# Kernel tuning notes

Hardware: AMD Instinct MI355X
Metric: run time of the kernel (lower is better)

The kernel has to match this reference:

```python
import jax, jax.numpy as jnp
import numpy as np

B = 8          # batch
S = 256        # nx+1 = ny+1 grid resolution
N = S * S      # number of DoFs per component
DIM = 2        # output vector dimension (= d_out)
W = 32         # FNO channel width
M1 = 12        # Fourier modes dim 1
M2 = 12        # Fourier modes dim 2
WF = 128       # final MLP hidden width
NL = 4         # number of Fourier layers
PADF = 8       # padding fraction denominator


def setup_inputs() -> dict:
    key = jax.random.key(0)
    ks = jax.random.split(key, 16)
    sc = 1.0 / (W * W)  # torch FNO spectral weight init scale
    return {
        "x": jax.random.normal(ks[0], (B, N), jnp.float32),
        "d2v_in": jax.random.permutation(ks[1], jnp.arange(N)),
        "v2d_out": jax.random.permutation(ks[2], jnp.arange(N)),
        "fc0_w": jax.random.normal(ks[3], (W, 3), jnp.float32) * 0.1,
        "fc0_b": jnp.zeros((W,), jnp.float32),
        "spec_w1r": jax.random.uniform(ks[4], (NL, W, W, M1, M2), jnp.float32) * sc,
        "spec_w1i": jax.random.uniform(ks[5], (NL, W, W, M1, M2), jnp.float32) * sc,
        "spec_w2r": jax.random.uniform(ks[6], (NL, W, W, M1, M2), jnp.float32) * sc,
        "spec_w2i": jax.random.uniform(ks[7], (NL, W, W, M1, M2), jnp.float32) * sc,
        "conv_w": jax.random.normal(ks[8], (NL, W, W), jnp.float32) * 0.05,
        "conv_b": jnp.zeros((NL, W), jnp.float32),
        "mlp_w1": jax.random.normal(ks[9], (WF, W), jnp.float32) * 0.05,
        "mlp_b1": jnp.zeros((WF,), jnp.float32),
        "mlp_w2": jax.random.normal(ks[10], (DIM, WF), jnp.float32) * 0.05,
        "mlp_b2": jnp.zeros((DIM,), jnp.float32),
    }


def _speconv(x, w1, w2):
    # x: (B, C, H, Wd) real; w1/w2: (C_in, C_out, M1, M2) complex64
    Bh, C, H, Wd = x.shape
    xft = jnp.fft.rfft2(x)  # (B, C, H, Wd//2+1)
    o1 = jnp.einsum('bixy,ioxy->boxy', xft[:, :, :M1, :M2], w1)
    o2 = jnp.einsum('bixy,ioxy->boxy', xft[:, :, -M1:, :M2], w2)
    out_ft = jnp.zeros((Bh, C, H, Wd // 2 + 1), jnp.complex64)
    out_ft = out_ft.at[:, :, :M1, :M2].set(o1).at[:, :, -M1:, :M2].set(o2)
    return jnp.fft.irfft2(out_ft, s=(H, Wd))


def reference(x, d2v_in, v2d_out, fc0_w, fc0_b,
              spec_w1r, spec_w1i, spec_w2r, spec_w2i,
              conv_w, conv_b, mlp_w1, mlp_b1, mlp_w2, mlp_b2):
    # DoF -> vertex gather and lift to image
    xg = x[:, d2v_in].reshape(B, 1, S, S)
    h = jnp.transpose(xg, (0, 2, 3, 1))  # (B, S, S, 1)
    # append normalized grid coordinates (get_grid2d)
    g = jnp.linspace(0.0, 1.0, S, dtype=jnp.float32)
    grid = jnp.stack(jnp.meshgrid(g, g, indexing='ij'), axis=-1)  # (S, S, 2)
    grid = jnp.broadcast_to(grid[None], (B, S, S, 2))
    h = jnp.concatenate([h, grid], axis=-1)
    # fc0 lifting
    h = h @ fc0_w.T + fc0_b              # (B, S, S, W)
    h = jnp.transpose(h, (0, 3, 1, 2))   # (B, W, S, S)
    # zero pad (non-periodic domain)
    p = S // PADF
    h = jnp.pad(h, ((0, 0), (0, 0), (0, p), (0, p)))  # (B, W, S+p, S+p)
    w1 = (spec_w1r + 1j * spec_w1i).astype(jnp.complex64)
    w2 = (spec_w2r + 1j * spec_w2i).astype(jnp.complex64)
    for l in range(NL):
        sp = _speconv(h, w1[l], w2[l])
        cv = jnp.einsum('bchw,oc->bohw', h, conv_w[l]) + conv_b[l][None, :, None, None]
        h = cv + sp
        if l != NL - 1:
            h = jax.nn.gelu(h, approximate=False)  # torch GELU default = exact erf
    # crop padding (s_outputspace=None path)
    h = h[..., :S, :S]
    # final two-layer MLP projection
    h = jnp.transpose(h, (0, 2, 3, 1))  # (B, S, S, W)
    h = jax.nn.gelu(h @ mlp_w1.T + mlp_b1, approximate=False) @ mlp_w2.T + mlp_b2
    h = jnp.transpose(h, (0, 3, 1, 2)).reshape(B, DIM, -1)  # (B, DIM, N)
    # vertex -> DoF scatter/gather and interleave components
    out = h[:, :, v2d_out]              # (B, DIM, N)
    out = jnp.transpose(out, (0, 2, 1)).reshape(B, -1)  # (B, N*DIM)
    return out
```

## Files before the change

kernel.cpp:

```cpp
#include <hip/hip_runtime.h>
#include <math.h>

#define S    256
#define Hp   288
#define C    32
#define KY   12
#define NK   24
#define Bn   8
#define PI_D 3.14159265358979323846264338327950288

#define SZ_TW  (NK*Hp*2)
#define OFF_TW 0
#define OFF_TWT (OFF_TW + SZ_TW)
#define SZ_TWT (Hp*KY*2)
#define OFF_H  (OFF_TWT + SZ_TWT)
#define SZ_H   (Bn*C*Hp*Hp)
#define OFF_Y  (OFF_H + SZ_H)
#define SZ_Y   (Bn*C*Hp*KY*2)
#define OFF_X  (OFF_Y + SZ_Y)
#define SZ_X   (Bn*C*NK*KY*2)
#define OFF_O  (OFF_X + 2*SZ_X)
#define SZ_O   SZ_X
#define OFF_Z  (OFF_O + SZ_O)
#define SZ_Z   (Bn*Hp*C*KY*2)
#define OFF_T  (OFF_Z + SZ_Z)
#define SZ_T   (Bn*S*S*2)

#define GELU(v) (0.5f*(v)*(1.0f+erff((v)*0.70710678118654752f)))
#define SCHED_FENCE() __builtin_amdgcn_sched_barrier(0)

__global__ void k_tw(float* __restrict__ tw, float* __restrict__ twT) {
    int i = blockIdx.x * 256 + threadIdx.x;
    if (i >= NK * Hp) return;
    int k = i / Hp, xx = i % Hp;
    int f = (k < KY) ? k : (k + 264);
    int m = (f * xx) % Hp;
    double th = (2.0 * PI_D * (double)m) / (double)Hp;
    float c = (float)cos(th), s = (float)sin(th);
    tw[2 * i] = c; tw[2 * i + 1] = s;
    if (k < KY) { twT[xx * 24 + 2 * k] = c; twT[xx * 24 + 2 * k + 1] = s; }
}

template<int Q>
__device__ __forceinline__ void embed_body(
        const float* __restrict__ xs, const float* __restrict__ twq,
        float* __restrict__ h, size_t rowbase, int o, int g,
        float w0, float w1, float w2, float bb, float gx,
        float* pr, float* pi) {
    #pragma unroll 1
    for (int c3 = 0; c3 < 3; ++c3) {
        int ybase = g * 36 + c3 * 12;
        int rowq  = (g & 1) * 36 + c3 * 12;
        float acc[12];
        #pragma unroll
        for (int j = 0; j < 12; ++j) {
            int y = ybase + j;
            acc[j] = (y < S) ? (w0 * xs[y < S ? y : 0] + w1 * gx + w2 * (y * (1.0f / 255.0f)) + bb) : 0.f;
        }
        float* hw = h + rowbase + (size_t)o * 82944 + ybase;
        #pragma unroll
        for (int q = 0; q < 3; ++q)
            *(float4*)&hw[4 * q] = make_float4(acc[4*q], acc[4*q+1], acc[4*q+2], acc[4*q+3]);
        SCHED_FENCE();
        #pragma unroll
        for (int jp = 0; jp < 6; ++jp) {
            #pragma unroll
            for (int u = 0; u < 2; ++u) {
                int j = jp * 2 + u;
                const float* tg = twq + (rowq + j) * 24;
                float tc[24];
                #pragma unroll
                for (int q = 0; q < 6; ++q) *(float4*)&tc[4 * q] = *(const float4*)&tg[4 * q];
                float v = acc[j];
                pr[0] += v;
                #pragma unroll
                for (int k = 1; k < 12; ++k) {
                    const int e = (k * Q) & 3;
                    float c = tc[2 * k], s = tc[2 * k + 1];
                    if      (e == 0) { pr[k] += v * c; pi[k] -= v * s; }
                    else if (e == 1) { pr[k] -= v * s; pi[k] -= v * c; }
                    else if (e == 2) { pr[k] -= v * c; pi[k] += v * s; }
                    else             { pr[k] += v * s; pi[k] += v * c; }
                }
            }
            SCHED_FENCE();
        }
    }
}

__global__ __launch_bounds__(256, 1) void k_embed(
        const float* __restrict__ xin, const int* __restrict__ d2v,
        const float* __restrict__ fw, const float* __restrict__ fb,
        const float* __restrict__ twT, float* __restrict__ h, float* __restrict__ Y) {
    __shared__ __align__(16) float xs[256];
    __shared__ __align__(16) float twq[1728];
    __shared__ __align__(16) float YP[3072];
    int x = blockIdx.x, b = blockIdx.y, tid = threadIdx.x;
    size_t rowbase = (size_t)b * 2654208 + (size_t)x * 288;
    if (x >= S) {
        for (int i = tid; i < 32 * 72; i += 256) {
            int c = i / 72, q = i % 72;
            *(float4*)&h[rowbase + (size_t)c * 82944 + q * 4] = make_float4(0, 0, 0, 0);
        }
        for (int i = tid; i < 768; i += 256)
            Y[((size_t)(b * 32 + i / 24) * 288 + x) * 24 + (i % 24)] = 0.f;
        return;
    }
    for (int i = tid; i < 432; i += 256)
        *(float4*)&twq[4 * i] = *(const float4*)&twT[4 * i];
    xs[tid] = xin[b * 65536 + d2v[x * 256 + tid]];
    int o = tid & 31, g = tid >> 5;
    float w0 = fw[o * 3], w1 = fw[o * 3 + 1], w2 = fw[o * 3 + 2], bb = fb[o];
    float gx = x * (1.0f / 255.0f);
    __syncthreads();
    float pr[12], pi[12];
    #pragma unroll
    for (int k = 0; k < 12; ++k) { pr[k] = 0.f; pi[k] = 0.f; }
    switch (tid >> 6) {
        case 0: embed_body<0>(xs, twq, h, rowbase, o, g, w0, w1, w2, bb, gx, pr, pi); break;
        case 1: embed_body<1>(xs, twq, h, rowbase, o, g, w0, w1, w2, bb, gx, pr, pi); break;
        case 2: embed_body<2>(xs, twq, h, rowbase, o, g, w0, w1, w2, bb, gx, pr, pi); break;
        default: embed_body<3>(xs, twq, h, rowbase, o, g, w0, w1, w2, bb, gx, pr, pi); break;
    }
    #pragma unroll
    for (int k = 0; k < 12; ++k) { pr[k] += __shfl_xor(pr[k], 32); pi[k] += __shfl_xor(pi[k], 32); }
    if ((tid & 32) == 0) {
        float* dst = YP + ((tid >> 6) * 32 + o) * 24;
        #pragma unroll
        for (int k = 0; k < 12; ++k) { dst[2 * k] = pr[k]; dst[2 * k + 1] = pi[k]; }
    }
    __syncthreads();
    for (int i = tid; i < 768; i += 256) {
        float s = YP[i] + YP[768 + i] + YP[1536 + i] + YP[2304 + i];
        Y[((size_t)(b * 32 + i / 24) * 288 + x) * 24 + (i % 24)] = s;
    }
}

__global__ __launch_bounds__(288) void k_dftx(const float* __restrict__ Y,
                                              const float* __restrict__ tw,
                                              float* __restrict__ X) {
    __shared__ __align__(16) float Ys[144 * 24];
    int c = blockIdx.x, b = blockIdx.y, half = blockIdx.z, tid = threadIdx.x;
    const float* Yb = Y + (size_t)(b * 32 + c) * 6912 + half * 3456;
    for (int i = tid; i < 864; i += 288)
        *(float4*)&Ys[4 * i] = *(const float4*)&Yb[4 * i];
    __syncthreads();
    int k = tid / 12, ky = tid % 12;
    const float* twk = tw + k * 576 + half * 288;
    float xr = 0.f, xi = 0.f;
    #pragma unroll 4
    for (int xx = 0; xx < 144; ++xx) {
        float yr = Ys[xx * 24 + 2 * ky], yi = Ys[xx * 24 + 2 * ky + 1];
        float cc = twk[2 * xx], ss = twk[2 * xx + 1];
        xr += yr * cc + yi * ss;
        xi += yi * cc - yr * ss;
    }
    size_t oo = (size_t)half * SZ_X + ((size_t)(b * 32 + c) * 288 + tid) * 2;
    X[oo] = xr; X[oo + 1] = xi;
}

__global__ void k_spec(const float* __restrict__ X,
                       const float* __restrict__ w1r, const float* __restrict__ w1i,
                       const float* __restrict__ w2r, const float* __restrict__ w2i,
                       float* __restrict__ O, int l) {
    int t = blockIdx.x * 256 + threadIdx.x;
    int ky = t % KY; int k = (t / KY) % NK; int o = (t / (NK * KY)) % C; int b = t / (C * NK * KY);
    int kk = (k < KY) ? k : (k - KY);
    const float* wr = (k < KY) ? w1r : w2r;
    const float* wi = (k < KY) ? w1i : w2i;
    size_t wbase = (size_t)l * C * C * 144 + (size_t)o * 144 + kk * 12 + ky;
    size_t xbase = (size_t)b * C * NK * KY * 2 + (k * KY + ky) * 2;
    float ar = 0.f, ai = 0.f;
    #pragma unroll 8
    for (int i = 0; i < C; ++i) {
        size_t xo = xbase + (size_t)i * NK * KY * 2;
        float xr = X[xo]     + X[SZ_X + xo];
        float xi = X[xo + 1] + X[SZ_X + xo + 1];
        float wrr = wr[wbase + (size_t)i * C * 144];
        float wii = wi[wbase + (size_t)i * C * 144];
        ar += xr * wrr - xi * wii;
        ai += xr * wii + xi * wrr;
    }
    size_t oo = (((size_t)b * C + o) * NK * KY + k * KY + ky) * 2;
    O[oo] = ar; O[oo + 1] = ai;
}

__global__ __launch_bounds__(384) void k_idftx(const float* __restrict__ O,
                                               const float* __restrict__ tw,
                                               float* __restrict__ Z) {
    int x0 = blockIdx.x * 32; int c = blockIdx.y, b = blockIdx.z;
    int row = threadIdx.x & 31, ky = threadIdx.x >> 5;
    int x = x0 + row;
    const float* Ob = O + ((size_t)(b * C + c)) * NK * KY * 2 + ky * 2;
    float zr = 0.f, zi = 0.f;
    #pragma unroll
    for (int k = 0; k < NK; ++k) {
        float orr = Ob[k * KY * 2], oii = Ob[k * KY * 2 + 1];
        float cc = tw[(k * Hp + x) * 2], ss = tw[(k * Hp + x) * 2 + 1];
        zr += orr * cc - oii * ss;
        zi += orr * ss + oii * cc;
    }
    size_t o = ((((size_t)b * Hp + x) * C + c) * KY + ky) * 2;
    Z[o] = zr; Z[o + 1] = zi;
}

__global__ __launch_bounds__(256, 1) void k_conv(
        float* __restrict__ h, const float* __restrict__ Z,
        const float* __restrict__ cw, const float* __restrict__ cb,
        const float* __restrict__ twT, float* __restrict__ Y,
        int l, int flags) {
    __shared__ __align__(16) float hs[32 * 292];
    __shared__ __align__(16) float twy[288 * 24];
    __shared__ __align__(16) float cws[32 * 33];
    __shared__ float cbs[32];
    int x = blockIdx.x, b = blockIdx.y, tid = threadIdx.x;
    size_t rowbase = (size_t)b * 2654208 + (size_t)x * 288;
    const float* hb = h + rowbase;
    for (int i = tid; i < 32 * 72; i += 256) {
        int c = i / 72, q = i % 72;
        *(float4*)&hs[c * 292 + q * 4] = *(const float4*)&hb[(size_t)c * 82944 + q * 4];
    }
    for (int i = tid; i < 1728; i += 256)
        *(float4*)&twy[4 * i] = *(const float4*)&twT[4 * i];
    for (int i = tid; i < 32 * 32; i += 256)
        cws[(i >> 5) * 33 + (i & 31)] = cw[l * 1024 + i];
    if (tid < 32) cbs[tid] = cb[l * 32 + tid];
    int o = tid & 31, g = tid >> 5;
    const float* Zr = Z + ((size_t)(b * 288 + x) * 32 + o) * 24;
    float zr[12], zi[12];
    #pragma unroll
    for (int q = 0; q < 6; ++q) {
        float4 zv = *(const float4*)&Zr[4 * q];
        zr[2*q] = zv.x; zi[2*q] = zv.y; zr[2*q+1] = zv.z; zi[2*q+1] = zv.w;
    }
    __syncthreads();
    float bias = cbs[o];
    float pr[12], pi[12];
    #pragma unroll
    for (int k = 0; k < 12; ++k) { pr[k] = 0.f; pi[k] = 0.f; }
    const int gelu_f = flags & 1, wy = flags & 2;
    #pragma unroll 1
    for (int c3 = 0; c3 < 3; ++c3) {
        int ybase = g * 36 + c3 * 12;
        float acc[12];
        #pragma unroll
        for (int j = 0; j < 12; ++j) acc[j] = bias;
        #pragma unroll 8
        for (int c = 0; c < 32; ++c) {
            float w = cws[o * 33 + c];
            const float* hr = &hs[c * 292 + ybase];
            float4 h0 = *(const float4*)&hr[0];
            float4 h1 = *(const float4*)&hr[4];
            float4 h2 = *(const float4*)&hr[8];
            acc[0] += h0.x * w; acc[1] += h0.y * w; acc[2]  += h0.z * w; acc[3]  += h0.w * w;
            acc[4] += h1.x * w; acc[5] += h1.y * w; acc[6]  += h1.z * w; acc[7]  += h1.w * w;
            acc[8] += h2.x * w; acc[9] += h2.y * w; acc[10] += h2.z * w; acc[11] += h2.w * w;
        }
        SCHED_FENCE();
        #pragma unroll
        for (int jp = 0; jp < 6; ++jp) {
            #pragma unroll
            for (int u = 0; u < 2; ++u) {
                int j = jp * 2 + u;
                int y = ybase + j;
                float tc[24];
                #pragma unroll
                for (int q = 0; q < 6; ++q) *(float4*)&tc[4 * q] = *(const float4*)&twy[y * 24 + 4 * q];
                float sp = zr[0] * tc[0] - zi[0] * tc[1];
                #pragma unroll
                for (int k = 1; k < 12; ++k) sp += 2.f * (zr[k] * tc[2*k] - zi[k] * tc[2*k+1]);
                float val = acc[j] + sp * (1.0f / 82944.0f);
                if (gelu_f) val = GELU(val);
                acc[j] = val;
                if (wy) {
                    #pragma unroll
                    for (int k = 0; k < 12; ++k) { pr[k] += val * tc[2*k]; pi[k] -= val * tc[2*k+1]; }
                }
            }
            SCHED_FENCE();
        }
        float* hw = h + rowbase + (size_t)o * 82944 + ybase;
        #pragma unroll
        for (int q = 0; q < 3; ++q)
            *(float4*)&hw[4 * q] = make_float4(acc[4*q], acc[4*q+1], acc[4*q+2], acc[4*q+3]);
        SCHED_FENCE();
    }
    if (wy) {
        #pragma unroll
        for (int k = 0; k < 12; ++k) { pr[k] += __shfl_xor(pr[k], 32); pi[k] += __shfl_xor(pi[k], 32); }
        __syncthreads();
        float* YP = twy;
        if ((tid & 32) == 0) {
            float* dst = YP + ((tid >> 6) * 32 + o) * 24;
            #pragma unroll
            for (int k = 0; k < 12; ++k) { dst[2 * k] = pr[k]; dst[2 * k + 1] = pi[k]; }
        }
        __syncthreads();
        for (int i = tid; i < 768; i += 256) {
            float s = YP[i] + YP[768 + i] + YP[1536 + i] + YP[2304 + i];
            Y[((size_t)(b * 32 + i / 24) * 288 + x) * 24 + (i % 24)] = s;
        }
    }
}

__global__ __launch_bounds__(256) void k_mlp(const float* __restrict__ h,
                                             const float* __restrict__ w1, const float* __restrict__ b1,
                                             const float* __restrict__ w2, const float* __restrict__ b2,
                                             float* __restrict__ tmp) {
    int bid = blockIdx.x;
    int b = bid >> 7;
    int x = ((bid & 127) << 1) + (threadIdx.x >> 7);
    int lane = threadIdx.x & 127;
    const float* hb = h + (size_t)b * 2654208 + (size_t)x * 288;
    float hc0[32], hc1[32];
    #pragma unroll
    for (int c = 0; c < 32; ++c) {
        hc0[c] = hb[(size_t)c * 82944 + lane];
        hc1[c] = hb[(size_t)c * 82944 + lane + 128];
    }
    float o00 = 0.f, o01 = 0.f, o10 = 0.f, o11 = 0.f;
    for (int f = 0; f < 128; ++f) {
        float a0 = b1[f], a1 = a0;
        #pragma unroll
        for (int c = 0; c < 32; ++c) {
            float w = w1[f * 32 + c];
            a0 += hc0[c] * w; a1 += hc1[c] * w;
        }
        float wa = w2[f], wb = w2[128 + f];
        float g0 = GELU(a0), g1 = GELU(a1);
        o00 += g0 * wa; o01 += g0 * wb;
        o10 += g1 * wa; o11 += g1 * wb;
    }
    float bb0 = b2[0], bb1 = b2[1];
    int p0 = x * 256 + lane;
    size_t base = (size_t)b * 65536;
    *(float2*)&tmp[(base + p0) * 2]       = make_float2(o00 + bb0, o01 + bb1);
    *(float2*)&tmp[(base + p0 + 128) * 2] = make_float2(o10 + bb0, o11 + bb1);
}

__global__ void k_scatter(const float* __restrict__ tmp, const int* __restrict__ v2d,
                          float* __restrict__ out) {
    int id = blockIdx.x * 256 + threadIdx.x;
    int b = id >> 16; int j = id & 65535;
    int p = v2d[j];
    const float2 v = *(const float2*)(tmp + ((size_t)(b << 16) + p) * 2);
    *(float2*)(out + (size_t)id * 2) = v;
}

extern "C" void kernel_launch(void* const* d_in, const int* in_sizes, int n_in,
                              void* d_out, int out_size, void* d_ws, size_t ws_size,
                              hipStream_t stream) {
    const float* xin   = (const float*)d_in[0];
    const int*   d2v   = (const int*)  d_in[1];
    const int*   v2d   = (const int*)  d_in[2];
    const float* fc0w  = (const float*)d_in[3];
    const float* fc0b  = (const float*)d_in[4];
    const float* w1r   = (const float*)d_in[5];
    const float* w1i   = (const float*)d_in[6];
    const float* w2r   = (const float*)d_in[7];
    const float* w2i   = (const float*)d_in[8];
    const float* cw    = (const float*)d_in[9];
    const float* cb    = (const float*)d_in[10];
    const float* mw1   = (const float*)d_in[11];
    const float* mb1   = (const float*)d_in[12];
    const float* mw2   = (const float*)d_in[13];
    const float* mb2   = (const float*)d_in[14];

    float* ws  = (float*)d_ws;
    float* TW  = ws + OFF_TW;
    float* TWT = ws + OFF_TWT;
    float* H   = ws + OFF_H;
    float* Y   = ws + OFF_Y;
    float* X   = ws + OFF_X;
    float* O   = ws + OFF_O;
    float* Z   = ws + OFF_Z;
    float* T   = ws + OFF_T;

    k_tw<<<(NK * Hp + 255) / 256, 256, 0, stream>>>(TW, TWT);
    k_embed<<<dim3(Hp, Bn), 256, 0, stream>>>(xin, d2v, fc0w, fc0b, TWT, H, Y);

    for (int l = 0; l < 4; ++l) {
        k_dftx<<<dim3(32, Bn, 2), 288, 0, stream>>>(Y, TW, X);
        k_spec<<<(Bn * C * NK * KY) / 256, 256, 0, stream>>>(X, w1r, w1i, w2r, w2i, O, l);
        k_idftx<<<dim3(9, 32, Bn), 384, 0, stream>>>(O, TW, Z);
        k_conv<<<dim3(Hp, Bn), 256, 0, stream>>>(H, Z, cw, cb, TWT, Y, l, (l != 3) ? 3 : 0);
    }

    k_mlp<<<1024, 256, 0, stream>>>(H, mw1, mb1, mw2, mb2, T);
    k_scatter<<<(Bn * S * S) / 256, 256, 0, stream>>>(T, v2d, (float*)d_out);
}
```

Baseline: 820.3 us.

## Fuse spectral mixing into inverse DFT, async LDS loads in conv, skip padded rows on last layer

Merges the spectral channel-mixing kernel into the inverse x-DFT kernel. Each block computes its 24x12 mode coefficients into shared memory, which removes one launch and the O buffer round trip, but the mixing work is now repeated in each of the 9 x-tiles. The conv kernel's H and twiddle tiles are loaded with global_load_lds async copies into an unpadded layout, and its reduction scratch moves from twy to hs. On the last layer the conv grid covers only the 256 unpadded rows, since the cropped padding is never read.

Result: no change. 812.8 us (-0.9%).

```diff
diff --git a/kernel.cpp b/kernel.cpp
--- a/kernel.cpp
+++ b/kernel.cpp
@@ -19,15 +19,22 @@
 #define SZ_Y   (Bn*C*Hp*KY*2)
 #define OFF_X  (OFF_Y + SZ_Y)
 #define SZ_X   (Bn*C*NK*KY*2)
-#define OFF_O  (OFF_X + 2*SZ_X)
-#define SZ_O   SZ_X
-#define OFF_Z  (OFF_O + SZ_O)
+#define OFF_Z  (OFF_X + 2*SZ_X)
 #define SZ_Z   (Bn*Hp*C*KY*2)
 #define OFF_T  (OFF_Z + SZ_Z)
 #define SZ_T   (Bn*S*S*2)
 
 #define GELU(v) (0.5f*(v)*(1.0f+erff((v)*0.70710678118654752f)))
 #define SCHED_FENCE() __builtin_amdgcn_sched_barrier(0)
+
+#if __has_builtin(__builtin_amdgcn_global_load_lds)
+#define HAS_ASYNC 1
+#define ASYNC_CP16(dst, src) \
+    __builtin_amdgcn_global_load_lds((const __attribute__((address_space(1))) void*)(src), \
+                                     (__attribute__((address_space(3))) void*)(dst), 16, 0, 0)
+#else
+#define HAS_ASYNC 0
+#endif
 
 __global__ void k_tw(float* __restrict__ tw, float* __restrict__ twT) {
     int i = blockIdx.x * 256 + threadIdx.x;
@@ -159,43 +166,40 @@
     X[oo] = xr; X[oo + 1] = xi;
 }
 
-__global__ void k_spec(const float* __restrict__ X,
-                       const float* __restrict__ w1r, const float* __restrict__ w1i,
-                       const float* __restrict__ w2r, const float* __restrict__ w2i,
-                       float* __restrict__ O, int l) {
-    int t = blockIdx.x * 256 + threadIdx.x;
-    int ky = t % KY; int k = (t / KY) % NK; int o = (t / (NK * KY)) % C; int b = t / (C * NK * KY);
-    int kk = (k < KY) ? k : (k - KY);
-    const float* wr = (k < KY) ? w1r : w2r;
-    const float* wi = (k < KY) ? w1i : w2i;
-    size_t wbase = (size_t)l * C * C * 144 + (size_t)o * 144 + kk * 12 + ky;
-    size_t xbase = (size_t)b * C * NK * KY * 2 + (k * KY + ky) * 2;
-    float ar = 0.f, ai = 0.f;
-    #pragma unroll 8
-    for (int i = 0; i < C; ++i) {
-        size_t xo = xbase + (size_t)i * NK * KY * 2;
-        float xr = X[xo]     + X[SZ_X + xo];
-        float xi = X[xo + 1] + X[SZ_X + xo + 1];
-        float wrr = wr[wbase + (size_t)i * C * 144];
-        float wii = wi[wbase + (size_t)i * C * 144];
-        ar += xr * wrr - xi * wii;
-        ai += xr * wii + xi * wrr;
-    }
-    size_t oo = (((size_t)b * C + o) * NK * KY + k * KY + ky) * 2;
-    O[oo] = ar; O[oo + 1] = ai;
-}
-
-__global__ __launch_bounds__(384) void k_idftx(const float* __restrict__ O,
-                                               const float* __restrict__ tw,
-                                               float* __restrict__ Z) {
-    int x0 = blockIdx.x * 32; int c = blockIdx.y, b = blockIdx.z;
-    int row = threadIdx.x & 31, ky = threadIdx.x >> 5;
+__global__ __launch_bounds__(384) void k_specidft(
+        const float* __restrict__ X,
+        const float* __restrict__ w1r, const float* __restrict__ w1i,
+        const float* __restrict__ w2r, const float* __restrict__ w2i,
+        const float* __restrict__ tw, float* __restrict__ Z, int l) {
+    __shared__ __align__(16) float Os[576];
+    int x0 = blockIdx.x * 32, c = blockIdx.y, b = blockIdx.z, tid = threadIdx.x;
+    if (tid < 288) {
+        int k = tid / 12, ky = tid % 12;
+        int kk = (k < KY) ? k : (k - KY);
+        const float* wr = (k < KY) ? w1r : w2r;
+        const float* wi = (k < KY) ? w1i : w2i;
+        size_t wbase = (size_t)l * 147456 + (size_t)c * 144 + kk * 12 + ky;
+        size_t xbase = (size_t)b * 18432 + (k * 12 + ky) * 2;
+        float ar = 0.f, ai = 0.f;
+        #pragma unroll 8
+        for (int i = 0; i < 32; ++i) {
+            size_t xo = xbase + (size_t)i * 576;
+            float xr = X[xo]     + X[SZ_X + xo];
+            float xi = X[xo + 1] + X[SZ_X + xo + 1];
+            float wrr = wr[wbase + (size_t)i * 4608];
+            float wii = wi[wbase + (size_t)i * 4608];
+            ar += xr * wrr - xi * wii;
+            ai += xr * wii + xi * wrr;
+        }
+        Os[2 * tid] = ar; Os[2 * tid + 1] = ai;
+    }
+    __syncthreads();
+    int row = tid & 31, ky = tid >> 5;
     int x = x0 + row;
-    const float* Ob = O + ((size_t)(b * C + c)) * NK * KY * 2 + ky * 2;
     float zr = 0.f, zi = 0.f;
     #pragma unroll
     for (int k = 0; k < NK; ++k) {
-        float orr = Ob[k * KY * 2], oii = Ob[k * KY * 2 + 1];
+        float orr = Os[(k * 12 + ky) * 2], oii = Os[(k * 12 + ky) * 2 + 1];
         float cc = tw[(k * Hp + x) * 2], ss = tw[(k * Hp + x) * 2 + 1];
         zr += orr * cc - oii * ss;
         zi += orr * ss + oii * cc;
@@ -209,19 +213,28 @@
         const float* __restrict__ cw, const float* __restrict__ cb,
         const float* __restrict__ twT, float* __restrict__ Y,
         int l, int flags) {
-    __shared__ __align__(16) float hs[32 * 292];
-    __shared__ __align__(16) float twy[288 * 24];
+    __shared__ __align__(16) float hs[9216];
+    __shared__ __align__(16) float twy[6912];
     __shared__ __align__(16) float cws[32 * 33];
     __shared__ float cbs[32];
     int x = blockIdx.x, b = blockIdx.y, tid = threadIdx.x;
     size_t rowbase = (size_t)b * 2654208 + (size_t)x * 288;
     const float* hb = h + rowbase;
-    for (int i = tid; i < 32 * 72; i += 256) {
-        int c = i / 72, q = i % 72;
-        *(float4*)&hs[c * 292 + q * 4] = *(const float4*)&hb[(size_t)c * 82944 + q * 4];
-    }
+#if HAS_ASYNC
+    #pragma unroll 1
+    for (int r = 0; r < 9; ++r) {
+        int i = r * 256 + tid;
+        ASYNC_CP16(&hs[4 * i], hb + (size_t)(i / 72) * 82944 + (i % 72) * 4);
+    }
+    #pragma unroll 1
+    for (int i = tid; i < 1728; i += 256)
+        ASYNC_CP16(&twy[4 * i], twT + 4 * i);
+#else
+    for (int i = tid; i < 2304; i += 256)
+        *(float4*)&hs[4 * i] = *(const float4*)&hb[(size_t)(i / 72) * 82944 + (i % 72) * 4];
     for (int i = tid; i < 1728; i += 256)
         *(float4*)&twy[4 * i] = *(const float4*)&twT[4 * i];
+#endif
     for (int i = tid; i < 32 * 32; i += 256)
         cws[(i >> 5) * 33 + (i & 31)] = cw[l * 1024 + i];
     if (tid < 32) cbs[tid] = cb[l * 32 + tid];
@@ -248,7 +261,7 @@
         #pragma unroll 8
         for (int c = 0; c < 32; ++c) {
             float w = cws[o * 33 + c];
-            const float* hr = &hs[c * 292 + ybase];
+            const float* hr = &hs[c * 288 + ybase];
             float4 h0 = *(const float4*)&hr[0];
             float4 h1 = *(const float4*)&hr[4];
             float4 h2 = *(const float4*)&hr[8];
@@ -289,7 +302,7 @@
         #pragma unroll
         for (int k = 0; k < 12; ++k) { pr[k] += __shfl_xor(pr[k], 32); pi[k] += __shfl_xor(pi[k], 32); }
         __syncthreads();
-        float* YP = twy;
+        float* YP = hs;
         if ((tid & 32) == 0) {
             float* dst = YP + ((tid >> 6) * 32 + o) * 24;
             #pragma unroll
@@ -372,7 +385,6 @@
     float* H   = ws + OFF_H;
     float* Y   = ws + OFF_Y;
     float* X   = ws + OFF_X;
-    float* O   = ws + OFF_O;
     float* Z   = ws + OFF_Z;
     float* T   = ws + OFF_T;
 
@@ -381,9 +393,8 @@
 
     for (int l = 0; l < 4; ++l) {
         k_dftx<<<dim3(32, Bn, 2), 288, 0, stream>>>(Y, TW, X);
-        k_spec<<<(Bn * C * NK * KY) / 256, 256, 0, stream>>>(X, w1r, w1i, w2r, w2i, O, l);
-        k_idftx<<<dim3(9, 32, Bn), 384, 0, stream>>>(O, TW, Z);
-        k_conv<<<dim3(Hp, Bn), 256, 0, stream>>>(H, Z, cw, cb, TWT, Y, l, (l != 3) ? 3 : 0);
+        k_specidft<<<dim3(9, 32, Bn), 384, 0, stream>>>(X, w1r, w1i, w2r, w2i, TW, Z, l);
+        k_conv<<<dim3((l != 3) ? Hp : S, Bn), 256, 0, stream>>>(H, Z, cw, cb, TWT, Y, l, (l != 3) ? 3 : 0);
     }
 
     k_mlp<<<1024, 256, 0, stream>>>(H, mw1, mb1, mw2, mb2, T);
```
